# Optimization experiments

Measured on AMD Instinct MI355X. Metric: run time of the kernel, lower is better.

## Reference

```python
import jax, jax.numpy as jnp
import numpy as np

B, T = 16, 2048
V, E, H, C = 32000, 512, 4, 3  # vocab, embed, heads, context (history 2 + current)
EPS = 1e-5


def setup_inputs() -> dict:
    key = jax.random.key(0)
    k0, k1, k2, k3, k4, k5, k6 = jax.random.split(key, 7)
    tokens = jax.random.randint(k0, (B, T), 0, V)
    embed_table = jax.random.normal(k1, (V, E), dtype=jnp.float32)
    pos = jax.random.normal(k2, (H, E, C), dtype=jnp.float32) * (1.0 / np.sqrt(H))
    ffn_w = jax.random.normal(k3, (E, E), dtype=jnp.float32) * (1.0 / np.sqrt(E))
    ffn_b = jax.random.normal(k4, (E,), dtype=jnp.float32) * 0.01
    ln_g = jnp.ones((E,), dtype=jnp.float32)
    ln_b = jnp.zeros((E,), dtype=jnp.float32)
    return {"tokens": tokens, "embed_table": embed_table, "pos": pos,
            "ffn_w": ffn_w, "ffn_b": ffn_b, "ln_g": ln_g, "ln_b": ln_b}


def reference(tokens, embed_table, pos, ffn_w, ffn_b, ln_g, ln_b):
    # embed lookup: [B, T, E]
    x = embed_table[tokens]
    # prepend zero history, extract sliding windows of size C: [B, T, C, E]
    x_cat = jnp.concatenate([jnp.zeros((B, C - 1, E), dtype=x.dtype), x], axis=1)
    x_win = jnp.stack([x_cat[:, i:i + T] for i in range(C)], axis=2)
    # multi-head positional scores: pos viewed as [H, C, E]
    pos_hce = jnp.transpose(pos, (0, 2, 1))  # [H, C, E]
    w = jnp.einsum('btce,hce->bthc', x_win, pos_hce)          # scores
    out = jnp.einsum('bthc,btce->bte', w, x_win) / (H * C)    # weighted sum
    # FFN (torch Linear: y = x @ W^T + b)
    out = out @ ffn_w.T + ffn_b
    # LayerNorm
    mu = jnp.mean(out, axis=-1, keepdims=True)
    var = jnp.mean(jnp.square(out - mu), axis=-1, keepdims=True)
    out = (out - mu) * jax.lax.rsqrt(var + EPS) * ln_g + ln_b
    # swish
    return out * jax.nn.sigmoid(out)
```

## Files before the change

### kernel.cpp

```cpp
#include <hip/hip_runtime.h>
#include <hip/hip_bf16.h>


#define Bq 16
#define Tq 2048
#define Eq 512
#define Cq 3
#define Hq 4
#define Vq 32000
#define Mq (Bq * Tq)
#define LN_EPS 1e-5f

typedef __attribute__((ext_vector_type(8))) short bf16x8;
typedef __attribute__((ext_vector_type(4))) float f32x4;

__device__ __forceinline__ unsigned short f2bf(float f) {
    unsigned int u = __float_as_uint(f);
    u += 0x7fffu + ((u >> 16) & 1u);
    return (unsigned short)(u >> 16);
}
__device__ __forceinline__ float bf2f(unsigned short h) {
    return __uint_as_float(((unsigned int)h) << 16);
}
__device__ __forceinline__ unsigned int cvt_pk_bf16(float lo, float hi) {
    unsigned int r;
    asm("v_cvt_pk_bf16_f32 %0, %1, %2" : "=v"(r) : "v"(lo), "v"(hi));
    return r;
}

__global__ void prep_kernel(const float* __restrict__ pos,
                            const float* __restrict__ ffn_w,
                            float* __restrict__ Pt,
                            unsigned short* __restrict__ Wb) {
    int i = blockIdx.x * blockDim.x + threadIdx.x;
    if (i < Cq * Eq) {
        int c = i / Eq, e = i % Eq;
        float s = 0.f;
#pragma unroll
        for (int h = 0; h < Hq; ++h) s += pos[(h * Eq + e) * Cq + c];
        Pt[i] = s;
    }
    for (int j = i; j < Eq * Eq; j += 16384) Wb[j] = f2bf(ffn_w[j]);
}

__global__ __launch_bounds__(256) void ep_kernel(const float* __restrict__ tbl,
                                                 const float* __restrict__ Pt,
                                                 float* __restrict__ EP) {
    const int wave = threadIdx.x >> 6;
    const int lane = threadIdx.x & 63;
    const int row = blockIdx.x * 4 + wave;
    const float4* rp = reinterpret_cast<const float4*>(tbl + (long)row * Eq + lane * 8);
    const float4 v0 = rp[0], v1 = rp[1];

    float s[Cq];
#pragma unroll
    for (int c = 0; c < Cq; ++c) {
        const float4* pp = reinterpret_cast<const float4*>(Pt + c * Eq + lane * 8);
        const float4 p0 = pp[0], p1 = pp[1];
        s[c] = v0.x * p0.x + v0.y * p0.y + v0.z * p0.z + v0.w * p0.w
             + v1.x * p1.x + v1.y * p1.y + v1.z * p1.z + v1.w * p1.w;
    }
#pragma unroll
    for (int m = 1; m < 64; m <<= 1) {
        s[0] += __shfl_xor(s[0], m, 64);
        s[1] += __shfl_xor(s[1], m, 64);
        s[2] += __shfl_xor(s[2], m, 64);
    }
    if (lane < 3) EP[(long)row * 4 + lane] = s[lane];
}

__global__ __launch_bounds__(256, 3) void xw_kernel(const float* __restrict__ tbl,
                                                    const unsigned short* __restrict__ Wb,
                                                    unsigned short* __restrict__ XW) {
    __shared__ __align__(16) char Abuf[2][8192];
    __shared__ __align__(16) char Bbuf[2][16384];

    const int tid = threadIdx.x;
    const int wave = tid >> 6;
    const int lane = tid & 63;
    const int lr = lane & 15;
    const int lg = lane >> 4;
    const int m0 = (int)blockIdx.y << 6;
    const int n0 = (int)blockIdx.x << 7;
    const int srow = tid >> 3;
    const int sslot = tid & 7;

    const char* WbB = reinterpret_cast<const char*>(Wb);
    float4 a_regs[2][2];

#define ISSUE_A(kb_)                                                               \
    {                                                                              \
        _Pragma("unroll")                                                          \
        for (int p = 0; p < 2; ++p) {                                              \
            const int row = p * 32 + srow;                                         \
            const int g = sslot ^ (row & 7);                                       \
            const float* s = tbl + (long)(m0 + row) * Eq + (kb_) * 64 + g * 8;     \
            a_regs[p][0] = reinterpret_cast<const float4*>(s)[0];                  \
            a_regs[p][1] = reinterpret_cast<const float4*>(s)[1];                  \
        }                                                                          \
    }
#define ISSUE_B(kb_, buf_)                                                         \
    {                                                                              \
        _Pragma("unroll")                                                          \
        for (int q = 0; q < 4; ++q) {                                              \
            const int row = q * 32 + srow;                                         \
            const int g = sslot ^ (row & 7);                                       \
            __builtin_amdgcn_global_load_lds(                                      \
                (const __attribute__((address_space(1))) void*)(WbB +              \
                    (long)(n0 + row) * 1024 + (kb_) * 128 + g * 16),               \
                (__attribute__((address_space(3))) void*)(Bbuf[buf_] + q * 4096 + tid * 16), \
                16, 0, 0);                                                         \
        }                                                                          \
    }
#define WRITE_A(buf_)                                                              \
    {                                                                              \
        _Pragma("unroll")                                                          \
        for (int p = 0; p < 2; ++p) {                                              \
            const int row = p * 32 + srow;                                         \
            uint4 o;                                                               \
            o.x = cvt_pk_bf16(a_regs[p][0].x, a_regs[p][0].y);                     \
            o.y = cvt_pk_bf16(a_regs[p][0].z, a_regs[p][0].w);                     \
            o.z = cvt_pk_bf16(a_regs[p][1].x, a_regs[p][1].y);                     \
            o.w = cvt_pk_bf16(a_regs[p][1].z, a_regs[p][1].w);                     \
            *reinterpret_cast<uint4*>(Abuf[buf_] + row * 128 + sslot * 16) = o;    \
        }                                                                          \
    }

    f32x4 acc[4][2];
#pragma unroll
    for (int i = 0; i < 4; ++i)
#pragma unroll
        for (int j = 0; j < 2; ++j) acc[i][j] = (f32x4){0.f, 0.f, 0.f, 0.f};

    ISSUE_A(0);
    ISSUE_B(0, 0);
    WRITE_A(0);
    __syncthreads();

#pragma unroll
    for (int kb = 0; kb < 8; ++kb) {
        const int cur = kb & 1;
        if (kb < 7) {
            ISSUE_A(kb + 1);
            ISSUE_B(kb + 1, cur ^ 1);
        }
#pragma unroll
        for (int ks = 0; ks < 2; ++ks) {
            bf16x8 af[4], bfv[2];
#pragma unroll
            for (int mf = 0; mf < 4; ++mf) {
                const int r = mf * 16 + lr;
                af[mf] = *reinterpret_cast<const bf16x8*>(
                    Abuf[cur] + r * 128 + ((ks * 64 + lg * 16) ^ ((r & 7) << 4)));
            }
#pragma unroll
            for (int nf = 0; nf < 2; ++nf) {
                const int c = wave * 32 + nf * 16 + lr;
                bfv[nf] = *reinterpret_cast<const bf16x8*>(
                    Bbuf[cur] + c * 128 + ((ks * 64 + lg * 16) ^ ((c & 7) << 4)));
            }
#pragma unroll
            for (int mf = 0; mf < 4; ++mf)
#pragma unroll
                for (int nf = 0; nf < 2; ++nf)
                    acc[mf][nf] = __builtin_amdgcn_mfma_f32_16x16x32_bf16(af[mf], bfv[nf], acc[mf][nf], 0, 0, 0);
        }
        if (kb < 7) {
            WRITE_A(cur ^ 1);
            __syncthreads();
        }
    }

#pragma unroll
    for (int mf = 0; mf < 4; ++mf)
#pragma unroll
        for (int i = 0; i < 4; ++i) {
            const int row = m0 + mf * 16 + (lg << 2) + i;
#pragma unroll
            for (int nf = 0; nf < 2; ++nf) {
                const int col = n0 + wave * 32 + nf * 16 + lr;
                XW[(long)row * Eq + col] = f2bf(acc[mf][nf][i]);
            }
        }
#undef ISSUE_A
#undef ISSUE_B
#undef WRITE_A
}

__global__ __launch_bounds__(512, 4) void gather_kernel(const int* __restrict__ tokens,
                                                        const unsigned short* __restrict__ XW,
                                                        const float* __restrict__ EP,
                                                        const float* __restrict__ bias,
                                                        const float* __restrict__ ln_g,
                                                        const float* __restrict__ ln_b,
                                                        float* __restrict__ out) {
    const int wave = threadIdx.x >> 6;
    const int lane = threadIdx.x & 63;
    const int tt = blockIdx.x * 8 + wave;
    const int t = tt & (Tq - 1);
    const int e0 = lane * 8;

    float v[8];
#pragma unroll
    for (int j = 0; j < 8; ++j) v[j] = 0.f;

#pragma unroll
    for (int c = 0; c < Cq; ++c) {
        if (t + c >= 2) {
            const int tok = tokens[tt + c - 2];
            const float s = EP[(long)tok * 4 + c];
            const bf16x8 xv = *reinterpret_cast<const bf16x8*>(XW + (long)tok * Eq + e0);
#pragma unroll
            for (int j = 0; j < 8; ++j)
                v[j] += s * bf2f((unsigned short)xv[j]);
        }
    }

    const float inv = 1.f / (Hq * Cq);
    const float4* bp = reinterpret_cast<const float4*>(bias + e0);
    const float4 b0 = bp[0], b1 = bp[1];
    float o[8];
    o[0] = v[0] * inv + b0.x; o[1] = v[1] * inv + b0.y;
    o[2] = v[2] * inv + b0.z; o[3] = v[3] * inv + b0.w;
    o[4] = v[4] * inv + b1.x; o[5] = v[5] * inv + b1.y;
    o[6] = v[6] * inv + b1.z; o[7] = v[7] * inv + b1.w;

    float sm = 0.f, sq = 0.f;
#pragma unroll
    for (int j = 0; j < 8; ++j) { sm += o[j]; sq += o[j] * o[j]; }
#pragma unroll
    for (int m = 1; m < 64; m <<= 1) {
        sm += __shfl_xor(sm, m, 64);
        sq += __shfl_xor(sq, m, 64);
    }
    const float mu = sm * (1.f / Eq);
    const float var = sq * (1.f / Eq) - mu * mu;
    const float rs = rsqrtf(var + LN_EPS);

    const float4* gp = reinterpret_cast<const float4*>(ln_g + e0);
    const float4* lp = reinterpret_cast<const float4*>(ln_b + e0);
    const float4 g0 = gp[0], g1 = gp[1];
    const float4 l0 = lp[0], l1 = lp[1];
    float gg[8] = {g0.x, g0.y, g0.z, g0.w, g1.x, g1.y, g1.z, g1.w};
    float ll[8] = {l0.x, l0.y, l0.z, l0.w, l1.x, l1.y, l1.z, l1.w};

    float4 r0, r1;
    float* rr0 = reinterpret_cast<float*>(&r0);
    float* rr1 = reinterpret_cast<float*>(&r1);
#pragma unroll
    for (int j = 0; j < 8; ++j) {
        float y = (o[j] - mu) * rs * gg[j] + ll[j];
        y = y / (1.f + __expf(-y));
        if (j < 4) rr0[j] = y; else rr1[j - 4] = y;
    }
    float4* op = reinterpret_cast<float4*>(out + (long)tt * Eq + e0);
    op[0] = r0;
    op[1] = r1;
}

extern "C" void kernel_launch(void* const* d_in, const int* in_sizes, int n_in,
                              void* d_out, int out_size, void* d_ws, size_t ws_size,
                              hipStream_t stream) {
    const int* tokens = (const int*)d_in[0];
    const float* tbl = (const float*)d_in[1];
    const float* pos = (const float*)d_in[2];
    const float* ffn_w = (const float*)d_in[3];
    const float* ffn_b = (const float*)d_in[4];
    const float* ln_g = (const float*)d_in[5];
    const float* ln_b = (const float*)d_in[6];
    float* out = (float*)d_out;

    char* ws = (char*)d_ws;
    float* Pt = (float*)ws;
    unsigned short* Wb = (unsigned short*)(ws + 16384);
    float* EP = (float*)(ws + (1 << 20));
    unsigned short* XW = (unsigned short*)(ws + (2 << 20));

    hipLaunchKernelGGL(prep_kernel, dim3(64), dim3(256), 0, stream, pos, ffn_w, Pt, Wb);
    hipLaunchKernelGGL(ep_kernel, dim3(Vq / 4), dim3(256), 0, stream, tbl, Pt, EP);
    hipLaunchKernelGGL(xw_kernel, dim3(4, Vq / 64), dim3(256), 0, stream, tbl, Wb, XW);
    hipLaunchKernelGGL(gather_kernel, dim3(Mq / 8), dim3(512), 0, stream,
                       tokens, XW, EP, ffn_b, ln_g, ln_b, out);
}
```

Before: 89.94 us.

## Fuse embedding score projection into XW GEMM, full-K A tile per block

Removes the separate ep_kernel and computes the per-row positional scores inside the XW GEMM kernel while loading the fp32 embedding rows. Each block now takes 32 vocab rows across the whole N=512 width, so each table row is read from HBM once rather than by four N-blocks plus the score kernel. The full K=512 A tile is converted to bf16 and held in LDS, and B fragments are read straight from global memory instead of being staged through LDS. The costs are the loss of the double-buffered pipeline and uncached B-operand loads from global or L2 inside the MFMA loop.

```diff
diff --git a/kernel.cpp b/kernel.cpp
--- a/kernel.cpp
+++ b/kernel.cpp
@@ -43,148 +43,107 @@
     for (int j = i; j < Eq * Eq; j += 16384) Wb[j] = f2bf(ffn_w[j]);
 }
 
-__global__ __launch_bounds__(256) void ep_kernel(const float* __restrict__ tbl,
-                                                 const float* __restrict__ Pt,
-                                                 float* __restrict__ EP) {
-    const int wave = threadIdx.x >> 6;
-    const int lane = threadIdx.x & 63;
-    const int row = blockIdx.x * 4 + wave;
-    const float4* rp = reinterpret_cast<const float4*>(tbl + (long)row * Eq + lane * 8);
-    const float4 v0 = rp[0], v1 = rp[1];
-
-    float s[Cq];
-#pragma unroll
-    for (int c = 0; c < Cq; ++c) {
-        const float4* pp = reinterpret_cast<const float4*>(Pt + c * Eq + lane * 8);
-        const float4 p0 = pp[0], p1 = pp[1];
-        s[c] = v0.x * p0.x + v0.y * p0.y + v0.z * p0.z + v0.w * p0.w
-             + v1.x * p1.x + v1.y * p1.y + v1.z * p1.z + v1.w * p1.w;
-    }
-#pragma unroll
-    for (int m = 1; m < 64; m <<= 1) {
-        s[0] += __shfl_xor(s[0], m, 64);
-        s[1] += __shfl_xor(s[1], m, 64);
-        s[2] += __shfl_xor(s[2], m, 64);
-    }
-    if (lane < 3) EP[(long)row * 4 + lane] = s[lane];
-}
-
-__global__ __launch_bounds__(256, 3) void xw_kernel(const float* __restrict__ tbl,
+__global__ __launch_bounds__(512, 4) void xw_kernel(const float* __restrict__ tbl,
                                                     const unsigned short* __restrict__ Wb,
-                                                    unsigned short* __restrict__ XW) {
-    __shared__ __align__(16) char Abuf[2][8192];
-    __shared__ __align__(16) char Bbuf[2][16384];
+                                                    const float* __restrict__ Pt,
+                                                    unsigned short* __restrict__ XW,
+                                                    float* __restrict__ EP) {
+    __shared__ __align__(16) char Albs[32 * 1024];
 
     const int tid = threadIdx.x;
     const int wave = tid >> 6;
     const int lane = tid & 63;
     const int lr = lane & 15;
     const int lg = lane >> 4;
-    const int m0 = (int)blockIdx.y << 6;
-    const int n0 = (int)blockIdx.x << 7;
-    const int srow = tid >> 3;
-    const int sslot = tid & 7;
-
-    const char* WbB = reinterpret_cast<const char*>(Wb);
-    float4 a_regs[2][2];
-
-#define ISSUE_A(kb_)                                                               \
-    {                                                                              \
-        _Pragma("unroll")                                                          \
-        for (int p = 0; p < 2; ++p) {                                              \
-            const int row = p * 32 + srow;                                         \
-            const int g = sslot ^ (row & 7);                                       \
-            const float* s = tbl + (long)(m0 + row) * Eq + (kb_) * 64 + g * 8;     \
-            a_regs[p][0] = reinterpret_cast<const float4*>(s)[0];                  \
-            a_regs[p][1] = reinterpret_cast<const float4*>(s)[1];                  \
-        }                                                                          \
-    }
-#define ISSUE_B(kb_, buf_)                                                         \
-    {                                                                              \
-        _Pragma("unroll")                                                          \
-        for (int q = 0; q < 4; ++q) {                                              \
-            const int row = q * 32 + srow;                                         \
-            const int g = sslot ^ (row & 7);                                       \
-            __builtin_amdgcn_global_load_lds(                                      \
-                (const __attribute__((address_space(1))) void*)(WbB +              \
-                    (long)(n0 + row) * 1024 + (kb_) * 128 + g * 16),               \
-                (__attribute__((address_space(3))) void*)(Bbuf[buf_] + q * 4096 + tid * 16), \
-                16, 0, 0);                                                         \
-        }                                                                          \
-    }
-#define WRITE_A(buf_)                                                              \
-    {                                                                              \
-        _Pragma("unroll")                                                          \
-        for (int p = 0; p < 2; ++p) {                                              \
-            const int row = p * 32 + srow;                                         \
-            uint4 o;                                                               \
-            o.x = cvt_pk_bf16(a_regs[p][0].x, a_regs[p][0].y);                     \
-            o.y = cvt_pk_bf16(a_regs[p][0].z, a_regs[p][0].w);                     \
-            o.z = cvt_pk_bf16(a_regs[p][1].x, a_regs[p][1].y);                     \
-            o.w = cvt_pk_bf16(a_regs[p][1].z, a_regs[p][1].w);                     \
-            *reinterpret_cast<uint4*>(Abuf[buf_] + row * 128 + sslot * 16) = o;    \
-        }                                                                          \
-    }
-
-    f32x4 acc[4][2];
-#pragma unroll
-    for (int i = 0; i < 4; ++i)
-#pragma unroll
-        for (int j = 0; j < 2; ++j) acc[i][j] = (f32x4){0.f, 0.f, 0.f, 0.f};
-
-    ISSUE_A(0);
-    ISSUE_B(0, 0);
-    WRITE_A(0);
+    const int m0 = (int)blockIdx.x << 5;
+
+#pragma unroll
+    for (int r = 0; r < 4; ++r) {
+        const int row = (r << 3) + wave;
+        const int swz = (row & 7) << 4;
+        const int kb16 = (lane << 4) ^ swz;
+        const int k0 = kb16 >> 1;
+        const float* src = tbl + (long)(m0 + row) * Eq + k0;
+        const float4 v0 = reinterpret_cast<const float4*>(src)[0];
+        const float4 v1 = reinterpret_cast<const float4*>(src)[1];
+
+        float s0 = 0.f, s1 = 0.f, s2 = 0.f;
+        {
+            const float4* p0 = reinterpret_cast<const float4*>(Pt + 0 * Eq + k0);
+            const float4* p1 = reinterpret_cast<const float4*>(Pt + 1 * Eq + k0);
+            const float4* p2 = reinterpret_cast<const float4*>(Pt + 2 * Eq + k0);
+            const float4 a0 = p0[0], a1 = p0[1];
+            const float4 b0 = p1[0], b1 = p1[1];
+            const float4 c0 = p2[0], c1 = p2[1];
+            s0 = v0.x * a0.x + v0.y * a0.y + v0.z * a0.z + v0.w * a0.w
+               + v1.x * a1.x + v1.y * a1.y + v1.z * a1.z + v1.w * a1.w;
+            s1 = v0.x * b0.x + v0.y * b0.y + v0.z * b0.z + v0.w * b0.w
+               + v1.x * b1.x + v1.y * b1.y + v1.z * b1.z + v1.w * b1.w;
+            s2 = v0.x * c0.x + v0.y * c0.y + v0.z * c0.z + v0.w * c0.w
+               + v1.x * c1.x + v1.y * c1.y + v1.z * c1.z + v1.w * c1.w;
+        }
+#pragma unroll
+        for (int m = 1; m < 64; m <<= 1) {
+            s0 += __shfl_xor(s0, m, 64);
+            s1 += __shfl_xor(s1, m, 64);
+            s2 += __shfl_xor(s2, m, 64);
+        }
+        if (lane < 3) {
+            const float sv = (lane == 0) ? s0 : (lane == 1) ? s1 : s2;
+            EP[(long)(m0 + row) * 4 + lane] = sv;
+        }
+
+        uint4 o;
+        o.x = cvt_pk_bf16(v0.x, v0.y);
+        o.y = cvt_pk_bf16(v0.z, v0.w);
+        o.z = cvt_pk_bf16(v1.x, v1.y);
+        o.w = cvt_pk_bf16(v1.z, v1.w);
+        *reinterpret_cast<uint4*>(Albs + row * 1024 + (lane << 4)) = o;
+    }
     __syncthreads();
 
+    const int n0 = wave << 6;
+    const short* Bp = reinterpret_cast<const short*>(Wb) + (long)n0 * Eq;
+
+    f32x4 acc[2][4];
+#pragma unroll
+    for (int i = 0; i < 2; ++i)
+#pragma unroll
+        for (int j = 0; j < 4; ++j) acc[i][j] = (f32x4){0.f, 0.f, 0.f, 0.f};
+
 #pragma unroll
     for (int kb = 0; kb < 8; ++kb) {
-        const int cur = kb & 1;
-        if (kb < 7) {
-            ISSUE_A(kb + 1);
-            ISSUE_B(kb + 1, cur ^ 1);
-        }
 #pragma unroll
         for (int ks = 0; ks < 2; ++ks) {
-            bf16x8 af[4], bfv[2];
-#pragma unroll
-            for (int mf = 0; mf < 4; ++mf) {
+            bf16x8 af[2], bfv[4];
+#pragma unroll
+            for (int nf = 0; nf < 4; ++nf)
+                bfv[nf] = *reinterpret_cast<const bf16x8*>(Bp + (nf * 16 + lr) * Eq + kb * 64 + ks * 32 + lg * 8);
+#pragma unroll
+            for (int mf = 0; mf < 2; ++mf) {
                 const int r = mf * 16 + lr;
                 af[mf] = *reinterpret_cast<const bf16x8*>(
-                    Abuf[cur] + r * 128 + ((ks * 64 + lg * 16) ^ ((r & 7) << 4)));
+                    Albs + r * 1024 + ((kb * 128 + ks * 64 + lg * 16) ^ ((r & 7) << 4)));
             }
 #pragma unroll
-            for (int nf = 0; nf < 2; ++nf) {
-                const int c = wave * 32 + nf * 16 + lr;
-                bfv[nf] = *reinterpret_cast<const bf16x8*>(
-                    Bbuf[cur] + c * 128 + ((ks * 64 + lg * 16) ^ ((c & 7) << 4)));
-            }
-#pragma unroll
-            for (int mf = 0; mf < 4; ++mf)
-#pragma unroll
-                for (int nf = 0; nf < 2; ++nf)
+            for (int mf = 0; mf < 2; ++mf)
+#pragma unroll
+                for (int nf = 0; nf < 4; ++nf)
                     acc[mf][nf] = __builtin_amdgcn_mfma_f32_16x16x32_bf16(af[mf], bfv[nf], acc[mf][nf], 0, 0, 0);
         }
-        if (kb < 7) {
-            WRITE_A(cur ^ 1);
-            __syncthreads();
-        }
-    }
-
-#pragma unroll
-    for (int mf = 0; mf < 4; ++mf)
+    }
+
+#pragma unroll
+    for (int mf = 0; mf < 2; ++mf)
 #pragma unroll
         for (int i = 0; i < 4; ++i) {
             const int row = m0 + mf * 16 + (lg << 2) + i;
 #pragma unroll
-            for (int nf = 0; nf < 2; ++nf) {
-                const int col = n0 + wave * 32 + nf * 16 + lr;
+            for (int nf = 0; nf < 4; ++nf) {
+                const int col = n0 + nf * 16 + lr;
                 XW[(long)row * Eq + col] = f2bf(acc[mf][nf][i]);
             }
         }
-#undef ISSUE_A
-#undef ISSUE_B
-#undef WRITE_A
 }
 
 __global__ __launch_bounds__(512, 4) void gather_kernel(const int* __restrict__ tokens,
@@ -277,8 +236,7 @@
     unsigned short* XW = (unsigned short*)(ws + (2 << 20));
 
     hipLaunchKernelGGL(prep_kernel, dim3(64), dim3(256), 0, stream, pos, ffn_w, Pt, Wb);
-    hipLaunchKernelGGL(ep_kernel, dim3(Vq / 4), dim3(256), 0, stream, tbl, Pt, EP);
-    hipLaunchKernelGGL(xw_kernel, dim3(4, Vq / 64), dim3(256), 0, stream, tbl, Wb, XW);
+    hipLaunchKernelGGL(xw_kernel, dim3(Vq / 32), dim3(512), 0, stream, tbl, Wb, Pt, XW, EP);
     hipLaunchKernelGGL(gather_kernel, dim3(Mq / 8), dim3(512), 0, stream,
                        tokens, XW, EP, ffn_b, ln_g, ln_b, out);
 }
```

Measured after the change: 100.5 us. 11.8% more time.
